# Optimization experiments

Hardware: AMD Instinct MI355X
Metric: run time of the kernel (lower is better)

The kernel has to match this reference:

```python
import jax, jax.numpy as jnp
import numpy as np

INIT_W = 0.1  # init_weight uniform range


def setup_inputs() -> dict:
    key = jax.random.key(0)
    kq, kk, kwq, kwk, ka = jax.random.split(key, 5)
    B, b, t_q, t_k = 2, 16, 64, 128
    qs = ks = nu = 512
    query = jax.random.normal(kq, (B, b, t_q, qs), dtype=jnp.float32)
    keys = jax.random.normal(kk, (B, b, t_k, ks), dtype=jnp.float32)
    # torch Linear weight layout: (out_features, in_features), per fusion slice
    Wq = (jax.random.uniform(kwq, (B, nu, qs), dtype=jnp.float32) * 2 - 1) * INIT_W
    Wk = (jax.random.uniform(kwk, (B, nu, ks), dtype=jnp.float32) * 2 - 1) * INIT_W
    linear_att = (jax.random.uniform(ka, (nu,), dtype=jnp.float32) * 2 - 1) * INIT_W
    return {"query": query, "keys": keys, "Wq": Wq, "Wk": Wk, "linear_att": linear_att}


def reference(query, keys, Wq, Wk, linear_att):
    # query: (B, b, t_q, query_size), keys: (B, b, t_k, key_size)
    # HFTA-fused linear projections (no bias): y = x @ W.T per fusion slice
    pq = jnp.einsum('Bbqi,Boi->Bbqo', query, Wq)   # (B, b, t_q, n)
    pk = jnp.einsum('Bbki,Boi->Bbko', keys, Wk)    # (B, b, t_k, n)
    # Bahdanau additive score: tanh(q + k) . v  (broadcast add over t_q x t_k)
    sum_qk = pq[:, :, :, None, :] + pk[:, :, None, :, :]   # (B, b, t_q, t_k, n)
    scores = jnp.einsum('Bbqkn,n->Bbqk', jnp.tanh(sum_qk), linear_att)
    scores_normalized = jax.nn.softmax(scores, axis=-1)    # (B, b, t_q, t_k)
    # context uses RAW keys (not projected)
    context = jnp.einsum('Bbqk,Bbkn->Bbqn', scores_normalized, keys)
    return context, scores_normalized
```

## Files before the change

### kernel.cpp

```cpp
#include <hip/hip_runtime.h>


#define DEV_INLINE __device__ __forceinline__

constexpr float C2    = 2.8853900817779268f;
constexpr float LOG2E = 1.4426950408889634f;

typedef _Float16 f16x8 __attribute__((ext_vector_type(8)));
typedef float    f32x16 __attribute__((ext_vector_type(16)));

DEV_INLINE unsigned int pk2(float a, float b) {
    auto h = __builtin_amdgcn_cvt_pkrtz(a, b);
    return __builtin_bit_cast(unsigned int, h);
}

DEV_INLINE float rcp_nr(float d) {
    float y = __builtin_bit_cast(float, 0x7EF311C3u - __builtin_bit_cast(unsigned int, d));
    y = y * (2.0f - d * y);
    y = y * (2.0f - d * y);
    return y;
}

#define GL2LDS16(g, l) __builtin_amdgcn_global_load_lds( \
    (const __attribute__((address_space(1))) void*)(g),  \
    (__attribute__((address_space(3))) void*)(l), 16, 0, 0)

DEV_INLINE float wave_rsum(float v) {
#pragma unroll
    for (int off = 32; off; off >>= 1) v += __shfl_xor(v, off, 64);
    return v;
}
DEV_INLINE float wave_rmax(float v) {
#pragma unroll
    for (int off = 32; off; off >>= 1) v = fmaxf(v, __shfl_xor(v, off, 64));
    return v;
}

__global__ __launch_bounds__(256)
void cvt_f16_kernel(const float* __restrict__ query, const float* __restrict__ keys,
                    const float* __restrict__ Wq,    const float* __restrict__ Wk,
                    const float* __restrict__ vatt,
                    uint2* __restrict__ dst, float* __restrict__ wtab)
{
    if (blockIdx.x == 4096) {
        const int t = threadIdx.x;
        wtab[t] = -2.f * vatt[t]; wtab[t + 256] = -2.f * vatt[t + 256];
        return;
    }
    const int i4 = blockIdx.x * 256 + threadIdx.x;
    const float* src; int base;
    if (i4 < 262144)      { src = query; base = 0; }
    else if (i4 < 786432) { src = keys;  base = 262144; }
    else if (i4 < 917504) { src = Wq;    base = 786432; }
    else                  { src = Wk;    base = 917504; }
    const float4 v = *reinterpret_cast<const float4*>(src + (size_t)(i4 - base) * 4);
    dst[i4] = make_uint2(pk2(v.x, v.y), pk2(v.z, v.w));
}

__global__ __launch_bounds__(256)
void proj_mfma_kernel(const _Float16* __restrict__ X16,
                      float* __restrict__ pqT, float* __restrict__ pkT)
{
    __shared__ __align__(16) unsigned char smem[24576];

    const int bid = (blockIdx.x & 7) * 48 + (blockIdx.x >> 3);

    int Bi, mt, tt, tkshift;
    const _Float16 *Wb, *Xb; float* Y;
    if (bid < 128) {
        Bi = bid >> 6; mt = (bid >> 4) & 3; tt = bid & 15;
        Xb = X16 + ((size_t)Bi * 1024 + tt * 64) * 512;
        Wb = X16 + 3145728 + (size_t)Bi * 262144 + (size_t)(mt * 128) * 512;
        Y = pqT; tkshift = 6;
    } else {
        const int b2 = bid - 128;
        Bi = b2 >> 7; mt = (b2 >> 5) & 3; tt = b2 & 31;
        Xb = X16 + 1048576 + ((size_t)Bi * 2048 + tt * 64) * 512;
        Wb = X16 + 3670016 + (size_t)Bi * 262144 + (size_t)(mt * 128) * 512;
        Y = pkT; tkshift = 7;
    }
    const int tid = threadIdx.x;

    auto srcoff = [](int u) {
        const int row = u >> 2, s = (u & 3) ^ ((row >> 1) & 3);
        return (size_t)row * 512 + s * 8;
    };
    const _Float16* gA0 = Wb + srcoff(tid);
    const _Float16* gA1 = Wb + srcoff(tid + 256);
    const _Float16* gB  = Xb + srcoff(tid);
    unsigned char* const ldsA0 = smem + tid * 16;
    unsigned char* const ldsA1 = smem + 4096 + tid * 16;
    unsigned char* const ldsB  = smem + 8192 + tid * 16;

    const int wid = tid >> 6, lane = tid & 63;
    const int wm = wid >> 1, wn = wid & 1;
    const int r31 = lane & 31, h = lane >> 5;
    auto lofs = [](int row, int slot) {
        return row * 64 + ((slot ^ ((row >> 1) & 3)) * 16);
    };
    const int rowA0 = wm * 64 + r31, rowA1 = rowA0 + 32, rowB = wn * 32 + r31;
    const int a00 = lofs(rowA0, h),     a01 = lofs(rowA0, 2 + h);
    const int a10 = lofs(rowA1, h),     a11 = lofs(rowA1, 2 + h);
    const int b0  = 8192 + lofs(rowB, h), b1 = 8192 + lofs(rowB, 2 + h);

    f32x16 acc0, acc1;
#pragma unroll
    for (int i = 0; i < 16; ++i) { acc0[i] = 0.f; acc1[i] = 0.f; }

    GL2LDS16(gA0, ldsA0);
    GL2LDS16(gA1, ldsA1);
    GL2LDS16(gB,  ldsB);
    asm volatile("s_waitcnt vmcnt(0)" ::: "memory");
    __builtin_amdgcn_s_barrier();

    for (int ks = 0; ks < 16; ++ks) {
        const int buf = ks & 1;
        if (ks < 15) {
            const int ko = (ks + 1) * 32, bo = (buf ^ 1) * 12288;
            GL2LDS16(gA0 + ko, ldsA0 + bo);
            GL2LDS16(gA1 + ko, ldsA1 + bo);
            GL2LDS16(gB  + ko, ldsB  + bo);
        }
        const unsigned char* sb = smem + buf * 12288;
        const f16x8 fa00 = *reinterpret_cast<const f16x8*>(sb + a00);
        const f16x8 fa01 = *reinterpret_cast<const f16x8*>(sb + a01);
        const f16x8 fa10 = *reinterpret_cast<const f16x8*>(sb + a10);
        const f16x8 fa11 = *reinterpret_cast<const f16x8*>(sb + a11);
        const f16x8 fb0  = *reinterpret_cast<const f16x8*>(sb + b0);
        const f16x8 fb1  = *reinterpret_cast<const f16x8*>(sb + b1);
        acc0 = __builtin_amdgcn_mfma_f32_32x32x16_f16(fa00, fb0, acc0, 0, 0, 0);
        acc0 = __builtin_amdgcn_mfma_f32_32x32x16_f16(fa01, fb1, acc0, 0, 0, 0);
        acc1 = __builtin_amdgcn_mfma_f32_32x32x16_f16(fa10, fb0, acc1, 0, 0, 0);
        acc1 = __builtin_amdgcn_mfma_f32_32x32x16_f16(fa11, fb1, acc1, 0, 0, 0);
        if (ks < 15) {
            asm volatile("s_waitcnt vmcnt(0)" ::: "memory");
            __builtin_amdgcn_s_barrier();
        }
    }

    const int TK = 1 << tkshift;
    const int trow = tt * 64 + wn * 32 + r31;
    const int slice = Bi * 16 + (trow >> tkshift);
    const int t = trow & (TK - 1);
    const int nf0 = mt * 128 + wm * 64 + 4 * h;
#pragma unroll
    for (int ab = 0; ab < 2; ++ab) {
        const f32x16 acc = ab ? acc1 : acc0;
#pragma unroll
        for (int reg = 0; reg < 16; ++reg) {
            const int nf = nf0 + ab * 32 + (reg & 3) + 8 * (reg >> 2);
            Y[((size_t)(slice * 512 + nf) << tkshift) + t] = acc[reg] * C2;
        }
    }
}

__global__ __launch_bounds__(1024)
void score_ctx_kernel(const float* __restrict__ pqT,
                      const float* __restrict__ pkT,
                      const float* __restrict__ wtab,
                      const float* __restrict__ keys,
                      float* __restrict__ sc_out,
                      float* __restrict__ ctx)
{
    const int xcd = blockIdx.x & 7, ix = blockIdx.x >> 3;
    const int slice = xcd * 4 + (ix >> 4);
    const int q0    = (ix & 15) * 4;
    const int tid   = threadIdx.x;
    const int k     = tid & 127;
    const int nh    = tid >> 7;

    __shared__ float partial[7][4][128];
    __shared__ __align__(16) float scQ[4][128];
    __shared__ __align__(16) float4 ctxp[4][4][128];
    __shared__ float wredm[8], wreds[8];

    const int wv = __builtin_amdgcn_readfirstlane(nh);
    const float* __restrict__ pqb = pqT + ((size_t)slice * 512 + wv * 64) * 64 + q0;
    const float* __restrict__ wb  = wtab + wv * 64;
    const float* __restrict__ pkp = pkT + ((size_t)slice * 512 + wv * 64) * 128 + k;

    float a0 = 0.f, a1 = 0.f, a2 = 0.f, a3 = 0.f;
#pragma unroll 8
    for (int n = 0; n < 64; ++n) {
        const float pk = pkp[(size_t)n * 128];
        const float4 pq = *reinterpret_cast<const float4*>(pqb + n * 64);
        const float w = wb[n];
        const float e0 = __builtin_amdgcn_exp2f(pq.x + pk) + 1.f;
        const float e1 = __builtin_amdgcn_exp2f(pq.y + pk) + 1.f;
        const float e2 = __builtin_amdgcn_exp2f(pq.z + pk) + 1.f;
        const float e3 = __builtin_amdgcn_exp2f(pq.w + pk) + 1.f;
        a0 = fmaf(w, rcp_nr(e0), a0);
        a1 = fmaf(w, rcp_nr(e1), a1);
        a2 = fmaf(w, __builtin_amdgcn_rcpf(e2), a2);
        a3 = fmaf(w, __builtin_amdgcn_rcpf(e3), a3);
    }
    if (nh) {
        partial[nh - 1][0][k] = a0; partial[nh - 1][1][k] = a1;
        partial[nh - 1][2][k] = a2; partial[nh - 1][3][k] = a3;
    }
    __syncthreads();
    if (!nh) {
        float s0 = a0, s1 = a1, s2 = a2, s3 = a3;
#pragma unroll
        for (int p = 0; p < 7; ++p) {
            s0 += partial[p][0][k]; s1 += partial[p][1][k];
            s2 += partial[p][2][k]; s3 += partial[p][3][k];
        }
        scQ[0][k] = s0; scQ[1][k] = s1; scQ[2][k] = s2; scQ[3][k] = s3;
    }
    __syncthreads();

    {
        const int j = nh & 3;
        float e = 0.f;
        if (tid < 512) {
            const float orig = scQ[j][k];
            const float m0 = wave_rmax(orig);
            if ((tid & 63) == 0) wredm[tid >> 6] = m0;
            e = orig;
        }
        __syncthreads();
        if (tid < 512) {
            const float m = fmaxf(wredm[2 * j], wredm[2 * j + 1]);
            e = __builtin_amdgcn_exp2f((e - m) * LOG2E);
            const float ss = wave_rsum(e);
            if ((tid & 63) == 0) wreds[tid >> 6] = ss;
        }
        __syncthreads();
        if (tid < 512) {
            const float s = wreds[2 * j] + wreds[2 * j + 1];
            const float p = e * __builtin_amdgcn_rcpf(s);
            sc_out[((size_t)slice * 64 + q0 + j) * 128 + k] = p;
            scQ[j][k] = p;
        }
    }
    __syncthreads();

    const int kg = nh, n4 = k;
    float4 acc0 = {0,0,0,0}, acc1 = {0,0,0,0}, acc2 = {0,0,0,0}, acc3 = {0,0,0,0};
    const float* __restrict__ kb = keys + (size_t)slice * 65536 + (size_t)(kg * 16) * 512 + n4 * 4;
#pragma unroll
    for (int r4 = 0; r4 < 4; ++r4) {
        const float4 pv0 = *reinterpret_cast<const float4*>(&scQ[0][kg * 16 + r4 * 4]);
        const float4 pv1 = *reinterpret_cast<const float4*>(&scQ[1][kg * 16 + r4 * 4]);
        const float4 pv2 = *reinterpret_cast<const float4*>(&scQ[2][kg * 16 + r4 * 4]);
        const float4 pv3 = *reinterpret_cast<const float4*>(&scQ[3][kg * 16 + r4 * 4]);
        const float pa[4][4] = {{pv0.x, pv0.y, pv0.z, pv0.w},
                                {pv1.x, pv1.y, pv1.z, pv1.w},
                                {pv2.x, pv2.y, pv2.z, pv2.w},
                                {pv3.x, pv3.y, pv3.z, pv3.w}};
#pragma unroll
        for (int rr = 0; rr < 4; ++rr) {
            const float4 kv = *reinterpret_cast<const float4*>(kb + (size_t)(r4 * 4 + rr) * 512);
            acc0.x = fmaf(pa[0][rr], kv.x, acc0.x); acc0.y = fmaf(pa[0][rr], kv.y, acc0.y);
            acc0.z = fmaf(pa[0][rr], kv.z, acc0.z); acc0.w = fmaf(pa[0][rr], kv.w, acc0.w);
            acc1.x = fmaf(pa[1][rr], kv.x, acc1.x); acc1.y = fmaf(pa[1][rr], kv.y, acc1.y);
            acc1.z = fmaf(pa[1][rr], kv.z, acc1.z); acc1.w = fmaf(pa[1][rr], kv.w, acc1.w);
            acc2.x = fmaf(pa[2][rr], kv.x, acc2.x); acc2.y = fmaf(pa[2][rr], kv.y, acc2.y);
            acc2.z = fmaf(pa[2][rr], kv.z, acc2.z); acc2.w = fmaf(pa[2][rr], kv.w, acc2.w);
            acc3.x = fmaf(pa[3][rr], kv.x, acc3.x); acc3.y = fmaf(pa[3][rr], kv.y, acc3.y);
            acc3.z = fmaf(pa[3][rr], kv.z, acc3.z); acc3.w = fmaf(pa[3][rr], kv.w, acc3.w);
        }
    }

    if (kg >= 4) {
        ctxp[kg - 4][0][n4] = acc0; ctxp[kg - 4][1][n4] = acc1;
        ctxp[kg - 4][2][n4] = acc2; ctxp[kg - 4][3][n4] = acc3;
    }
    __syncthreads();
    if (kg < 4) {
        const float4 o0 = ctxp[kg][0][n4], o1 = ctxp[kg][1][n4];
        const float4 o2 = ctxp[kg][2][n4], o3 = ctxp[kg][3][n4];
        acc0.x += o0.x; acc0.y += o0.y; acc0.z += o0.z; acc0.w += o0.w;
        acc1.x += o1.x; acc1.y += o1.y; acc1.z += o1.z; acc1.w += o1.w;
        acc2.x += o2.x; acc2.y += o2.y; acc2.z += o2.z; acc2.w += o2.w;
        acc3.x += o3.x; acc3.y += o3.y; acc3.z += o3.z; acc3.w += o3.w;
    }
    __syncthreads();
    if (kg == 2 || kg == 3) {
        ctxp[kg - 2][0][n4] = acc0; ctxp[kg - 2][1][n4] = acc1;
        ctxp[kg - 2][2][n4] = acc2; ctxp[kg - 2][3][n4] = acc3;
    }
    __syncthreads();
    if (kg < 2) {
        const float4 o0 = ctxp[kg][0][n4], o1 = ctxp[kg][1][n4];
        const float4 o2 = ctxp[kg][2][n4], o3 = ctxp[kg][3][n4];
        acc0.x += o0.x; acc0.y += o0.y; acc0.z += o0.z; acc0.w += o0.w;
        acc1.x += o1.x; acc1.y += o1.y; acc1.z += o1.z; acc1.w += o1.w;
        acc2.x += o2.x; acc2.y += o2.y; acc2.z += o2.z; acc2.w += o2.w;
        acc3.x += o3.x; acc3.y += o3.y; acc3.z += o3.z; acc3.w += o3.w;
    }
    __syncthreads();
    if (kg == 1) {
        ctxp[0][0][n4] = acc0; ctxp[0][1][n4] = acc1;
        ctxp[0][2][n4] = acc2; ctxp[0][3][n4] = acc3;
    }
    __syncthreads();
    if (kg == 0) {
        const float4 o0 = ctxp[0][0][n4], o1 = ctxp[0][1][n4];
        const float4 o2 = ctxp[0][2][n4], o3 = ctxp[0][3][n4];
        acc0.x += o0.x; acc0.y += o0.y; acc0.z += o0.z; acc0.w += o0.w;
        acc1.x += o1.x; acc1.y += o1.y; acc1.z += o1.z; acc1.w += o1.w;
        acc2.x += o2.x; acc2.y += o2.y; acc2.z += o2.z; acc2.w += o2.w;
        acc3.x += o3.x; acc3.y += o3.y; acc3.z += o3.z; acc3.w += o3.w;
        float* cb = ctx + ((size_t)slice * 64 + q0) * 512 + n4 * 4;
        *reinterpret_cast<float4*>(cb)             = acc0;
        *reinterpret_cast<float4*>(cb + 512)       = acc1;
        *reinterpret_cast<float4*>(cb + 2 * 512)   = acc2;
        *reinterpret_cast<float4*>(cb + 3 * 512)   = acc3;
    }
}

extern "C" void kernel_launch(void* const* d_in, const int* in_sizes, int n_in,
                              void* d_out, int out_size, void* d_ws, size_t ws_size,
                              hipStream_t stream)
{
    const float* query = (const float*)d_in[0];
    const float* keys  = (const float*)d_in[1];
    const float* Wq    = (const float*)d_in[2];
    const float* Wk    = (const float*)d_in[3];
    const float* vatt  = (const float*)d_in[4];

    float* ctx_out = (float*)d_out;
    float* sc_out  = ctx_out + (size_t)32 * 64 * 512;

    float* pqT = (float*)d_ws;
    float* pkT = pqT + (size_t)32 * 512 * 64;
    _Float16* X16 = (_Float16*)((char*)d_ws + 12 * 1024 * 1024);
    float* wtab = (float*)((char*)d_ws + 20 * 1024 * 1024);

    cvt_f16_kernel<<<dim3(4097), 256, 0, stream>>>(query, keys, Wq, Wk, vatt,
                                                   (uint2*)X16, wtab);
    proj_mfma_kernel<<<dim3(384), 256, 0, stream>>>(X16, pqT, pkT);
    score_ctx_kernel<<<dim3(512), 1024, 0, stream>>>(pqT, pkT, wtab, keys, sc_out, ctx_out);
}
```

Measured before the change: 53.89 us.

## Fuse fp32-to-fp16 conversion into projection GEMM and drop convert kernel

Removes the separate conversion kernel that wrote fp16 copies of query, keys and weights to workspace. The projection kernel now streams fp32 tiles into LDS (doubled LDS footprint, new swizzle) and packs them to fp16 fragments in registers before the MFMAs. The -2*v scaling is moved from a precomputed table to a single multiply on the reduced score. This saves a kernel launch and a full read-write pass over the inputs, at the cost of twice the global-to-LDS traffic and extra conversion instructions in the GEMM loop.

```diff
diff --git a/kernel.cpp b/kernel.cpp
--- a/kernel.cpp
+++ b/kernel.cpp
@@ -12,6 +12,13 @@
 DEV_INLINE unsigned int pk2(float a, float b) {
     auto h = __builtin_amdgcn_cvt_pkrtz(a, b);
     return __builtin_bit_cast(unsigned int, h);
+}
+
+DEV_INLINE f16x8 mkfrag(float4 c0, float4 c1) {
+    uint4 u;
+    u.x = pk2(c0.x, c0.y); u.y = pk2(c0.z, c0.w);
+    u.z = pk2(c1.x, c1.y); u.w = pk2(c1.z, c1.w);
+    return __builtin_bit_cast(f16x8, u);
 }
 
 DEV_INLINE float rcp_nr(float d) {
@@ -37,97 +44,88 @@
 }
 
 __global__ __launch_bounds__(256)
-void cvt_f16_kernel(const float* __restrict__ query, const float* __restrict__ keys,
-                    const float* __restrict__ Wq,    const float* __restrict__ Wk,
-                    const float* __restrict__ vatt,
-                    uint2* __restrict__ dst, float* __restrict__ wtab)
+void proj_mfma_kernel(const float* __restrict__ query, const float* __restrict__ keys,
+                      const float* __restrict__ Wq,    const float* __restrict__ Wk,
+                      float* __restrict__ pqT,         float* __restrict__ pkT)
 {
-    if (blockIdx.x == 4096) {
-        const int t = threadIdx.x;
-        wtab[t] = -2.f * vatt[t]; wtab[t + 256] = -2.f * vatt[t + 256];
-        return;
-    }
-    const int i4 = blockIdx.x * 256 + threadIdx.x;
-    const float* src; int base;
-    if (i4 < 262144)      { src = query; base = 0; }
-    else if (i4 < 786432) { src = keys;  base = 262144; }
-    else if (i4 < 917504) { src = Wq;    base = 786432; }
-    else                  { src = Wk;    base = 917504; }
-    const float4 v = *reinterpret_cast<const float4*>(src + (size_t)(i4 - base) * 4);
-    dst[i4] = make_uint2(pk2(v.x, v.y), pk2(v.z, v.w));
-}
-
-__global__ __launch_bounds__(256)
-void proj_mfma_kernel(const _Float16* __restrict__ X16,
-                      float* __restrict__ pqT, float* __restrict__ pkT)
-{
-    __shared__ __align__(16) unsigned char smem[24576];
+    __shared__ __align__(16) unsigned char smem[49152];
 
     const int bid = (blockIdx.x & 7) * 48 + (blockIdx.x >> 3);
 
     int Bi, mt, tt, tkshift;
-    const _Float16 *Wb, *Xb; float* Y;
+    const float *Ab, *Bb; float* Y;
     if (bid < 128) {
         Bi = bid >> 6; mt = (bid >> 4) & 3; tt = bid & 15;
-        Xb = X16 + ((size_t)Bi * 1024 + tt * 64) * 512;
-        Wb = X16 + 3145728 + (size_t)Bi * 262144 + (size_t)(mt * 128) * 512;
+        Bb = query + ((size_t)Bi * 1024 + tt * 64) * 512;
+        Ab = Wq + (size_t)Bi * 262144 + (size_t)(mt * 128) * 512;
         Y = pqT; tkshift = 6;
     } else {
         const int b2 = bid - 128;
         Bi = b2 >> 7; mt = (b2 >> 5) & 3; tt = b2 & 31;
-        Xb = X16 + 1048576 + ((size_t)Bi * 2048 + tt * 64) * 512;
-        Wb = X16 + 3670016 + (size_t)Bi * 262144 + (size_t)(mt * 128) * 512;
+        Bb = keys + ((size_t)Bi * 2048 + tt * 64) * 512;
+        Ab = Wk + (size_t)Bi * 262144 + (size_t)(mt * 128) * 512;
         Y = pkT; tkshift = 7;
     }
     const int tid = threadIdx.x;
 
     auto srcoff = [](int u) {
-        const int row = u >> 2, s = (u & 3) ^ ((row >> 1) & 3);
-        return (size_t)row * 512 + s * 8;
+        const int row = u >> 3, s = (u & 7) ^ (row & 7);
+        return (size_t)row * 512 + s * 4;
     };
-    const _Float16* gA0 = Wb + srcoff(tid);
-    const _Float16* gA1 = Wb + srcoff(tid + 256);
-    const _Float16* gB  = Xb + srcoff(tid);
-    unsigned char* const ldsA0 = smem + tid * 16;
-    unsigned char* const ldsA1 = smem + 4096 + tid * 16;
-    unsigned char* const ldsB  = smem + 8192 + tid * 16;
+    const float* gA0 = Ab + srcoff(tid);
+    const float* gA1 = Ab + srcoff(tid + 256);
+    const float* gA2 = Ab + srcoff(tid + 512);
+    const float* gA3 = Ab + srcoff(tid + 768);
+    const float* gB0 = Bb + srcoff(tid);
+    const float* gB1 = Bb + srcoff(tid + 256);
+    unsigned char* const lA0 = smem + tid * 16;
+    unsigned char* const lA1 = smem + 4096  + tid * 16;
+    unsigned char* const lA2 = smem + 8192  + tid * 16;
+    unsigned char* const lA3 = smem + 12288 + tid * 16;
+    unsigned char* const lB0 = smem + 16384 + tid * 16;
+    unsigned char* const lB1 = smem + 20480 + tid * 16;
 
     const int wid = tid >> 6, lane = tid & 63;
     const int wm = wid >> 1, wn = wid & 1;
     const int r31 = lane & 31, h = lane >> 5;
     auto lofs = [](int row, int slot) {
-        return row * 64 + ((slot ^ ((row >> 1) & 3)) * 16);
+        return row * 128 + ((slot ^ (row & 7)) * 16);
     };
     const int rowA0 = wm * 64 + r31, rowA1 = rowA0 + 32, rowB = wn * 32 + r31;
-    const int a00 = lofs(rowA0, h),     a01 = lofs(rowA0, 2 + h);
-    const int a10 = lofs(rowA1, h),     a11 = lofs(rowA1, 2 + h);
-    const int b0  = 8192 + lofs(rowB, h), b1 = 8192 + lofs(rowB, 2 + h);
+    const int a00_0 = lofs(rowA0, 2 * h),     a00_1 = lofs(rowA0, 2 * h + 1);
+    const int a01_0 = lofs(rowA0, 4 + 2 * h), a01_1 = lofs(rowA0, 5 + 2 * h);
+    const int a10_0 = lofs(rowA1, 2 * h),     a10_1 = lofs(rowA1, 2 * h + 1);
+    const int a11_0 = lofs(rowA1, 4 + 2 * h), a11_1 = lofs(rowA1, 5 + 2 * h);
+    const int b0_0  = 16384 + lofs(rowB, 2 * h),     b0_1 = 16384 + lofs(rowB, 2 * h + 1);
+    const int b1_0  = 16384 + lofs(rowB, 4 + 2 * h), b1_1 = 16384 + lofs(rowB, 5 + 2 * h);
 
     f32x16 acc0, acc1;
 #pragma unroll
     for (int i = 0; i < 16; ++i) { acc0[i] = 0.f; acc1[i] = 0.f; }
 
-    GL2LDS16(gA0, ldsA0);
-    GL2LDS16(gA1, ldsA1);
-    GL2LDS16(gB,  ldsB);
+    GL2LDS16(gA0, lA0); GL2LDS16(gA1, lA1);
+    GL2LDS16(gA2, lA2); GL2LDS16(gA3, lA3);
+    GL2LDS16(gB0, lB0); GL2LDS16(gB1, lB1);
     asm volatile("s_waitcnt vmcnt(0)" ::: "memory");
     __builtin_amdgcn_s_barrier();
 
     for (int ks = 0; ks < 16; ++ks) {
         const int buf = ks & 1;
         if (ks < 15) {
-            const int ko = (ks + 1) * 32, bo = (buf ^ 1) * 12288;
-            GL2LDS16(gA0 + ko, ldsA0 + bo);
-            GL2LDS16(gA1 + ko, ldsA1 + bo);
-            GL2LDS16(gB  + ko, ldsB  + bo);
-        }
-        const unsigned char* sb = smem + buf * 12288;
-        const f16x8 fa00 = *reinterpret_cast<const f16x8*>(sb + a00);
-        const f16x8 fa01 = *reinterpret_cast<const f16x8*>(sb + a01);
-        const f16x8 fa10 = *reinterpret_cast<const f16x8*>(sb + a10);
-        const f16x8 fa11 = *reinterpret_cast<const f16x8*>(sb + a11);
-        const f16x8 fb0  = *reinterpret_cast<const f16x8*>(sb + b0);
-        const f16x8 fb1  = *reinterpret_cast<const f16x8*>(sb + b1);
+            const int ko = (ks + 1) * 32, bo = (buf ^ 1) * 24576;
+            GL2LDS16(gA0 + ko, lA0 + bo); GL2LDS16(gA1 + ko, lA1 + bo);
+            GL2LDS16(gA2 + ko, lA2 + bo); GL2LDS16(gA3 + ko, lA3 + bo);
+            GL2LDS16(gB0 + ko, lB0 + bo); GL2LDS16(gB1 + ko, lB1 + bo);
+        }
+        const unsigned char* sb = smem + buf * 24576;
+#define LD4(off) (*reinterpret_cast<const float4*>(sb + (off)))
+        const f16x8 fa00 = mkfrag(LD4(a00_0), LD4(a00_1));
+        const f16x8 fa01 = mkfrag(LD4(a01_0), LD4(a01_1));
+        const f16x8 fa10 = mkfrag(LD4(a10_0), LD4(a10_1));
+        const f16x8 fa11 = mkfrag(LD4(a11_0), LD4(a11_1));
+        const f16x8 fb0  = mkfrag(LD4(b0_0),  LD4(b0_1));
+        const f16x8 fb1  = mkfrag(LD4(b1_0),  LD4(b1_1));
+#undef LD4
         acc0 = __builtin_amdgcn_mfma_f32_32x32x16_f16(fa00, fb0, acc0, 0, 0, 0);
         acc0 = __builtin_amdgcn_mfma_f32_32x32x16_f16(fa01, fb1, acc0, 0, 0, 0);
         acc1 = __builtin_amdgcn_mfma_f32_32x32x16_f16(fa10, fb0, acc1, 0, 0, 0);
@@ -157,7 +155,7 @@
 __global__ __launch_bounds__(1024)
 void score_ctx_kernel(const float* __restrict__ pqT,
                       const float* __restrict__ pkT,
-                      const float* __restrict__ wtab,
+                      const float* __restrict__ vatt,
                       const float* __restrict__ keys,
                       float* __restrict__ sc_out,
                       float* __restrict__ ctx)
@@ -176,7 +174,7 @@
 
     const int wv = __builtin_amdgcn_readfirstlane(nh);
     const float* __restrict__ pqb = pqT + ((size_t)slice * 512 + wv * 64) * 64 + q0;
-    const float* __restrict__ wb  = wtab + wv * 64;
+    const float* __restrict__ vb  = vatt + wv * 64;
     const float* __restrict__ pkp = pkT + ((size_t)slice * 512 + wv * 64) * 128 + k;
 
     float a0 = 0.f, a1 = 0.f, a2 = 0.f, a3 = 0.f;
@@ -184,15 +182,15 @@
     for (int n = 0; n < 64; ++n) {
         const float pk = pkp[(size_t)n * 128];
         const float4 pq = *reinterpret_cast<const float4*>(pqb + n * 64);
-        const float w = wb[n];
+        const float v = vb[n];
         const float e0 = __builtin_amdgcn_exp2f(pq.x + pk) + 1.f;
         const float e1 = __builtin_amdgcn_exp2f(pq.y + pk) + 1.f;
         const float e2 = __builtin_amdgcn_exp2f(pq.z + pk) + 1.f;
         const float e3 = __builtin_amdgcn_exp2f(pq.w + pk) + 1.f;
-        a0 = fmaf(w, rcp_nr(e0), a0);
-        a1 = fmaf(w, rcp_nr(e1), a1);
-        a2 = fmaf(w, __builtin_amdgcn_rcpf(e2), a2);
-        a3 = fmaf(w, __builtin_amdgcn_rcpf(e3), a3);
+        a0 = fmaf(v, rcp_nr(e0), a0);
+        a1 = fmaf(v, rcp_nr(e1), a1);
+        a2 = fmaf(v, __builtin_amdgcn_rcpf(e2), a2);
+        a3 = fmaf(v, __builtin_amdgcn_rcpf(e3), a3);
     }
     if (nh) {
         partial[nh - 1][0][k] = a0; partial[nh - 1][1][k] = a1;
@@ -206,7 +204,8 @@
             s0 += partial[p][0][k]; s1 += partial[p][1][k];
             s2 += partial[p][2][k]; s3 += partial[p][3][k];
         }
-        scQ[0][k] = s0; scQ[1][k] = s1; scQ[2][k] = s2; scQ[3][k] = s3;
+        scQ[0][k] = -2.f * s0; scQ[1][k] = -2.f * s1;
+        scQ[2][k] = -2.f * s2; scQ[3][k] = -2.f * s3;
     }
     __syncthreads();
 
@@ -326,11 +325,7 @@
 
     float* pqT = (float*)d_ws;
     float* pkT = pqT + (size_t)32 * 512 * 64;
-    _Float16* X16 = (_Float16*)((char*)d_ws + 12 * 1024 * 1024);
-    float* wtab = (float*)((char*)d_ws + 20 * 1024 * 1024);
-
-    cvt_f16_kernel<<<dim3(4097), 256, 0, stream>>>(query, keys, Wq, Wk, vatt,
-                                                   (uint2*)X16, wtab);
-    proj_mfma_kernel<<<dim3(384), 256, 0, stream>>>(X16, pqT, pkT);
-    score_ctx_kernel<<<dim3(512), 1024, 0, stream>>>(pqT, pkT, wtab, keys, sc_out, ctx_out);
-}
+
+    proj_mfma_kernel<<<dim3(384), 256, 0, stream>>>(query, keys, Wq, Wk, pqT, pkT);
+    score_ctx_kernel<<<dim3(512), 1024, 0, stream>>>(pqT, pkT, vatt, keys, sc_out, ctx_out);
+}
```

Measured after the change: 54.86 us. Within noise of the previous version (+1.8%).
